# Kernel tuning notes

Measured on AMD Instinct MI355X. Metric: run time of the kernel, lower is better.

The kernel has to match this reference:

```python
import jax, jax.numpy as jnp
import numpy as np

B, C, H, W = 16, 256, 64, 64

def setup_inputs() -> dict:
    key = jax.random.key(0)
    ks = jax.random.split(key, 4)
    scale = 1.0 / np.sqrt(C)
    return {
        "x": jax.random.normal(ks[0], (B, C, H, W), dtype=jnp.float32),
        "w1": jax.random.normal(ks[1], (C, C), dtype=jnp.float32) * scale,
        "b1": jnp.zeros((C,), dtype=jnp.float32),
        "w2": jax.random.normal(ks[2], (C, C), dtype=jnp.float32) * scale,
        "b2": jnp.zeros((C,), dtype=jnp.float32),
        "w3": jax.random.normal(ks[3], (C, C), dtype=jnp.float32) * scale,
        "b3": jnp.zeros((C,), dtype=jnp.float32),
    }

def reference(x, w1, b1, w2, b2, w3, b3):
    b, c, h, w = x.shape
    n = h * w
    # 1x1 convs == per-pixel linear maps over channels; w has shape [C_out, C_in]
    def proj(wt, bias):
        return jnp.einsum('bchw,oc->bohw', x, wt) + bias[None, :, None, None]
    v = proj(w1, b1).reshape(b, c, n).transpose(0, 2, 1)   # [B, N, C]
    q = proj(w2, b2).reshape(b, c, n)                      # [B, C, N]
    k = proj(w3, b3).reshape(b, c, n)                      # [B, C, N]
    weight = jnp.einsum('bcn,bdn->bcd', q, k)              # [B, C, C]
    # global softmax over the entire flattened C*C matrix per batch element
    weight = jax.nn.softmax(weight.reshape(b, -1), axis=1).reshape(b, c, c)
    out = jnp.einsum('bnc,bcd->bdn', v, weight)            # [B, C, N]
    return out.reshape(x.shape)
```

## Files before the change

### kernel.cpp

```cpp
#include <hip/hip_runtime.h>


typedef unsigned short u16;
typedef __attribute__((ext_vector_type(8))) short short8;
typedef __attribute__((ext_vector_type(4))) float floatx4;

__device__ __forceinline__ u16 f2b(float f) {
  union { float f; unsigned int u; } v; v.f = f;
  unsigned int u = v.u;
  return (u16)((u + 0x7fffu + ((u >> 16) & 1u)) >> 16);
}
__device__ __forceinline__ float b2f(u16 h) {
  union { unsigned int u; float f; } v; v.u = ((unsigned int)h) << 16;
  return v.f;
}
__device__ __forceinline__ unsigned int cvt_pk_bf16(float lo, float hi) {
  unsigned int r;
  asm("v_cvt_pk_bf16_f32 %0, %1, %2" : "=v"(r) : "v"(lo), "v"(hi));
  return r;
}
__device__ __forceinline__ void gload_lds16(const u16* g, u16* l) {
  __builtin_amdgcn_global_load_lds(
      (const __attribute__((address_space(1))) unsigned int*)(const void*)g,
      (__attribute__((address_space(3))) unsigned int*)(void*)l, 16, 0, 0);
}

__global__ __launch_bounds__(256) void prep_w_kernel(
    const float* __restrict__ w1, const float* __restrict__ w2, const float* __restrict__ w3,
    u16* __restrict__ W1Th, u16* __restrict__ W2h, u16* __restrict__ W2l,
    u16* __restrict__ W3h, u16* __restrict__ W3l, float* __restrict__ xsum) {
  const int blk = blockIdx.x, t = threadIdx.x;
  if (blk == 576) {
#pragma unroll
    for (int i = 0; i < 16; ++i) xsum[t + i * 256] = 0.f;
    return;
  }
  if (blk < 64) {
    __shared__ float tile[32][33];
    const int e0 = (blk & 7) * 32, c0 = (blk >> 3) * 32;
    const int tx = t & 31, ty = t >> 5;
#pragma unroll
    for (int i = 0; i < 4; ++i)
      tile[ty + i * 8][tx] = w1[(c0 + ty + i * 8) * 256 + e0 + tx];
    __syncthreads();
#pragma unroll
    for (int i = 0; i < 4; ++i)
      W1Th[(e0 + ty + i * 8) * 256 + c0 + tx] = f2b(tile[tx][ty + i * 8]);
  } else {
    const int i = (blk - 64) * 256 + t;
    const int e = i & 0xffff;
    const float f = (i >> 16) ? w3[e] : w2[e];
    u16 h = f2b(f);
    if (i >> 16) { W3h[e] = h; W3l[e] = f2b(f - b2f(h)); }
    else         { W2h[e] = h; W2l[e] = f2b(f - b2f(h)); }
  }
}

__device__ __forceinline__ void stage8(const float4 a, const float4 b,
                                       u16* dH, u16* dL, float& xa) {
  const float f[8] = {a.x, a.y, a.z, a.w, b.x, b.y, b.z, b.w};
  union { unsigned int w[4]; uint4 q; } uh, ul;
#pragma unroll
  for (int i = 0; i < 4; ++i) {
    const unsigned int h = cvt_pk_bf16(f[2 * i], f[2 * i + 1]);
    uh.w[i] = h;
    union { unsigned int u; float ff; } h0, h1;
    h0.u = h << 16;
    h1.u = h & 0xffff0000u;
    ul.w[i] = cvt_pk_bf16(f[2 * i] - h0.ff, f[2 * i + 1] - h1.ff);
    xa += f[2 * i] + f[2 * i + 1];
  }
  *(uint4*)dH = uh.q;
  *(uint4*)dL = ul.q;
}

__global__ __launch_bounds__(512, 4) void gram_kernel(
    const float* __restrict__ x, float* __restrict__ Gp, float* __restrict__ xsum) {
  __shared__ u16 lH[2][256 * 32], lL[2][256 * 32];
  const int b = blockIdx.x >> 5, s = (blockIdx.x >> 1) & 15, mh = blockIdx.x & 1;
  const float* Xb = x + (long)b * 1048576 + s * 256;
  const int t = threadIdx.x;
  const int lane = t & 63, wave = t >> 6;
  const int quad = lane >> 4, l16 = lane & 15;
  const int wml = (wave & 1) * 64 + mh * 128;
  const int wn = (wave >> 1) * 64;
  const int r0 = t >> 2, qc = (t & 3) * 8;
  const int r1 = r0 + 128;
  const int wq = (((t & 3) ^ ((r0 >> 1) & 3))) * 8;
  const int rq = ((quad ^ ((l16 >> 1) & 3))) * 8;
  const int ph = s & 7;
  floatx4 acc[4][4] = {};
  float xa0 = 0.f, xa1 = 0.f;
  float4 p[4];
  {
    const long k0 = ph * 32;
    p[0] = *(const float4*)(Xb + (long)r0 * 4096 + k0 + qc);
    p[1] = *(const float4*)(Xb + (long)r0 * 4096 + k0 + qc + 4);
    p[2] = *(const float4*)(Xb + (long)r1 * 4096 + k0 + qc);
    p[3] = *(const float4*)(Xb + (long)r1 * 4096 + k0 + qc + 4);
  }
  stage8(p[0], p[1], lH[0] + r0 * 32 + wq, lL[0] + r0 * 32 + wq, xa0);
  stage8(p[2], p[3], lH[0] + r1 * 32 + wq, lL[0] + r1 * 32 + wq, xa1);
  __syncthreads();
  for (int kb = 0; kb < 8; ++kb) {
    const int cur = kb & 1, nxt = cur ^ 1;
    if (kb < 7) {
      const long kk = (long)(((kb + 1 + ph) & 7) * 32);
      p[0] = *(const float4*)(Xb + (long)r0 * 4096 + kk + qc);
      p[1] = *(const float4*)(Xb + (long)r0 * 4096 + kk + qc + 4);
      p[2] = *(const float4*)(Xb + (long)r1 * 4096 + kk + qc);
      p[3] = *(const float4*)(Xb + (long)r1 * 4096 + kk + qc + 4);
    }
    const u16* cH = lH[cur];
    const u16* cL = lL[cur];
    short8 ah[4], al[4];
#pragma unroll
    for (int i = 0; i < 4; ++i) {
      ah[i] = *(const short8*)(cH + (wml + i * 16 + l16) * 32 + rq);
      al[i] = *(const short8*)(cL + (wml + i * 16 + l16) * 32 + rq);
    }
#pragma unroll
    for (int j = 0; j < 4; ++j) {
      const short8 bh = *(const short8*)(cH + (wn + j * 16 + l16) * 32 + rq);
      const short8 bl = *(const short8*)(cL + (wn + j * 16 + l16) * 32 + rq);
#pragma unroll
      for (int i = 0; i < 4; ++i) {
        acc[i][j] = __builtin_amdgcn_mfma_f32_16x16x32_bf16(ah[i], bh, acc[i][j], 0, 0, 0);
        acc[i][j] = __builtin_amdgcn_mfma_f32_16x16x32_bf16(ah[i], bl, acc[i][j], 0, 0, 0);
        acc[i][j] = __builtin_amdgcn_mfma_f32_16x16x32_bf16(al[i], bh, acc[i][j], 0, 0, 0);
      }
    }
    if (kb < 7) {
      stage8(p[0], p[1], lH[nxt] + r0 * 32 + wq, lL[nxt] + r0 * 32 + wq, xa0);
      stage8(p[2], p[3], lH[nxt] + r1 * 32 + wq, lL[nxt] + r1 * 32 + wq, xa1);
    }
    __syncthreads();
  }
  if (mh == 0) {
    float v = xa0;
    v += __shfl_xor(v, 1);
    v += __shfl_xor(v, 2);
    if ((t & 3) == 0) atomicAdd(&xsum[b * 256 + r0], v);
    v = xa1;
    v += __shfl_xor(v, 1);
    v += __shfl_xor(v, 2);
    if ((t & 3) == 0) atomicAdd(&xsum[b * 256 + r1], v);
  }
  float* G = Gp + ((long)b * 16 + s) * 65536;
#pragma unroll
  for (int i = 0; i < 4; ++i) {
    const int row0 = wml + i * 16 + quad * 4;
#pragma unroll
    for (int j = 0; j < 4; ++j) {
      const int col = wn + j * 16 + l16;
#pragma unroll
      for (int r = 0; r < 4; ++r)
        G[(long)(row0 + r) * 256 + col] = acc[i][j][r];
    }
  }
}

__global__ __launch_bounds__(256) void reduce_g_kernel(
    const float* __restrict__ Gp, u16* __restrict__ Gh, u16* __restrict__ Gl) {
  const long e = ((long)blockIdx.x * 256 + threadIdx.x) * 4;
  const long base = ((e >> 16) << 20) + (e & 65535);
  float4 s = {0.f, 0.f, 0.f, 0.f};
#pragma unroll
  for (int i = 0; i < 16; ++i) {
    const float4 v = *(const float4*)(Gp + base + (long)i * 65536);
    s.x += v.x; s.y += v.y; s.z += v.z; s.w += v.w;
  }
  union { u16 h[4]; uint2 q; } oh, ol;
  const float sv[4] = {s.x, s.y, s.z, s.w};
#pragma unroll
  for (int c = 0; c < 4; ++c) {
    const u16 h = f2b(sv[c]);
    oh.h[c] = h;
    ol.h[c] = f2b(sv[c] - b2f(h));
  }
  *(uint2*)(Gh + e) = oh.q;
  *(uint2*)(Gl + e) = ol.q;
}

template <bool X3, int EPI>
__global__ __launch_bounds__(256) void gemm_small(
    const u16* __restrict__ Ah, const u16* __restrict__ Al,
    const u16* __restrict__ Bh, const u16* __restrict__ Bl,
    long aBatch, long bBatch, long oBatch,
    float* __restrict__ outF, u16* __restrict__ outH, u16* __restrict__ outL,
    const float* __restrict__ S2, const float* __restrict__ S3,
    const float* __restrict__ b2v, const float* __restrict__ b3v,
    float* __restrict__ bm, float* __restrict__ bs) {
  constexpr int LW = 264;
  __shared__ u16 smem[(X3 ? 4 : 2) * 64 * LW];
  __shared__ float rm[4], rs[4];
  u16* lAh = smem;
  u16* lBh = smem + 64 * LW;
  u16* lAl = X3 ? (smem + 2 * 64 * LW) : nullptr;
  u16* lBl = X3 ? (smem + 3 * 64 * LW) : nullptr;
  const int b = blockIdx.z;
  const int tm = blockIdx.x & 3, tn = blockIdx.x >> 2;
  const u16* Ahb = Ah + (long)b * aBatch + (long)tm * 64 * 256;
  const u16* Bhb = Bh + (long)b * bBatch + (long)tn * 64 * 256;
  const int t = threadIdx.x;
  const int lane = t & 63, wave = t >> 6;
  const int quad = lane >> 4, l16 = lane & 15;
  const int wm = (wave & 1) * 32, wn = (wave >> 1) * 32;
  const int r = t >> 2, c4 = t & 3;
  {
    uint4 tmp[8];
#pragma unroll
    for (int j = 0; j < 8; ++j)
      tmp[j] = *(const uint4*)(Ahb + (long)r * 256 + (c4 + 4 * j) * 8);
#pragma unroll
    for (int j = 0; j < 8; ++j)
      *(uint4*)(lAh + r * LW + (c4 + 4 * j) * 8) = tmp[j];
#pragma unroll
    for (int j = 0; j < 8; ++j)
      tmp[j] = *(const uint4*)(Bhb + (long)r * 256 + (c4 + 4 * j) * 8);
#pragma unroll
    for (int j = 0; j < 8; ++j)
      *(uint4*)(lBh + r * LW + (c4 + 4 * j) * 8) = tmp[j];
    if (X3) {
      const u16* Alb = Al + (long)b * aBatch + (long)tm * 64 * 256;
      const u16* Blb = Bl + (long)b * bBatch + (long)tn * 64 * 256;
#pragma unroll
      for (int j = 0; j < 8; ++j)
        tmp[j] = *(const uint4*)(Alb + (long)r * 256 + (c4 + 4 * j) * 8);
#pragma unroll
      for (int j = 0; j < 8; ++j)
        *(uint4*)(lAl + r * LW + (c4 + 4 * j) * 8) = tmp[j];
#pragma unroll
      for (int j = 0; j < 8; ++j)
        tmp[j] = *(const uint4*)(Blb + (long)r * 256 + (c4 + 4 * j) * 8);
#pragma unroll
      for (int j = 0; j < 8; ++j)
        *(uint4*)(lBl + r * LW + (c4 + 4 * j) * 8) = tmp[j];
    }
  }
  __syncthreads();
  floatx4 acc[2][2] = {};
#pragma unroll
  for (int kk = 0; kk < 8; ++kk) {
    const int co = kk * 32 + quad * 8;
    short8 afh[2], bfh[2];
#pragma unroll
    for (int i = 0; i < 2; ++i) {
      afh[i] = *(const short8*)(lAh + (wm + i * 16 + l16) * LW + co);
      bfh[i] = *(const short8*)(lBh + (wn + i * 16 + l16) * LW + co);
    }
    if (X3) {
      short8 afl[2], bfl[2];
#pragma unroll
      for (int i = 0; i < 2; ++i) {
        afl[i] = *(const short8*)(lAl + (wm + i * 16 + l16) * LW + co);
        bfl[i] = *(const short8*)(lBl + (wn + i * 16 + l16) * LW + co);
      }
#pragma unroll
      for (int i = 0; i < 2; ++i)
#pragma unroll
        for (int j = 0; j < 2; ++j) {
          acc[i][j] = __builtin_amdgcn_mfma_f32_16x16x32_bf16(afh[i], bfh[j], acc[i][j], 0, 0, 0);
          acc[i][j] = __builtin_amdgcn_mfma_f32_16x16x32_bf16(afh[i], bfl[j], acc[i][j], 0, 0, 0);
          acc[i][j] = __builtin_amdgcn_mfma_f32_16x16x32_bf16(afl[i], bfh[j], acc[i][j], 0, 0, 0);
        }
    } else {
#pragma unroll
      for (int i = 0; i < 2; ++i)
#pragma unroll
        for (int j = 0; j < 2; ++j)
          acc[i][j] = __builtin_amdgcn_mfma_f32_16x16x32_bf16(afh[i], bfh[j], acc[i][j], 0, 0, 0);
    }
  }
  const long obase = (long)b * oBatch;
  if (EPI == 3) {
    float vals[2][2][4];
    float vmax = -3.4e38f;
#pragma unroll
    for (int i = 0; i < 2; ++i) {
      const int mb = tm * 64 + wm + i * 16 + quad * 4;
#pragma unroll
      for (int rr = 0; rr < 4; ++rr) {
        const int d = mb + rr;
        const float c1 = b3v[d];
        const float c0 = S3[b * 256 + d] + 4096.f * c1;
#pragma unroll
        for (int j = 0; j < 2; ++j) {
          const int a = tn * 64 + wn + j * 16 + l16;
          const float raw = acc[i][j][rr];
          const float vv = raw + b2v[a] * c0 + c1 * S2[b * 256 + a];
          vals[i][j][rr] = vv;
          vmax = fmaxf(vmax, vv);
          outF[obase + (long)d * 256 + a] = raw;
        }
      }
    }
    for (int o = 32; o; o >>= 1) vmax = fmaxf(vmax, __shfl_xor(vmax, o));
    if (lane == 0) rm[wave] = vmax;
    __syncthreads();
    const float bmax = fmaxf(fmaxf(rm[0], rm[1]), fmaxf(rm[2], rm[3]));
    float se = 0.f;
#pragma unroll
    for (int i = 0; i < 2; ++i)
#pragma unroll
      for (int j = 0; j < 2; ++j)
#pragma unroll
        for (int rr = 0; rr < 4; ++rr) se += __expf(vals[i][j][rr] - bmax);
    for (int o = 32; o; o >>= 1) se += __shfl_xor(se, o);
    if (lane == 0) rs[wave] = se;
    __syncthreads();
    if (t == 0) {
      bm[b * 16 + blockIdx.x] = bmax;
      bs[b * 16 + blockIdx.x] = rs[0] + rs[1] + rs[2] + rs[3];
    }
    return;
  }
#pragma unroll
  for (int i = 0; i < 2; ++i) {
    const int mb = tm * 64 + wm + i * 16 + quad * 4;
#pragma unroll
    for (int j = 0; j < 2; ++j) {
      const int n = tn * 64 + wn + j * 16 + l16;
#pragma unroll
      for (int rr = 0; rr < 4; ++rr) {
        const float v = acc[i][j][rr];
        const long idx = obase + (long)(mb + rr) * 256 + n;
        if (EPI == 0) {
          outF[idx] = v;
        } else if (EPI == 1) {
          u16 h = f2b(v);
          outH[idx] = h;
          outL[idx] = f2b(v - b2f(h));
        } else {
          outH[idx] = f2b(v);
        }
      }
    }
  }
}

__global__ __launch_bounds__(512, 2) void gemm_out(
    const u16* __restrict__ Mh, const float* __restrict__ x,
    const float* __restrict__ bb, float* __restrict__ out) {
  __shared__ u16 lA[2][256 * 32];
  __shared__ u16 lB[128 * 40];
  const int b = blockIdx.z;
  const int tn = blockIdx.x;
  const u16* Ab = Mh + (long)b * 65536;
  const float* Xb = x + (long)b * 1048576 + tn * 128;
  const int t = threadIdx.x;
  const int lane = t & 63, wave = t >> 6;
  const int quad = lane >> 4, l16 = lane & 15;
  const int wm = (wave & 3) * 64;
  const int wn = (wave >> 2) * 64;
  const int erp = (t >> 5) * 2;
  const int n0 = t & 31;
  const int ra = t >> 2;
  const int sc = ((t & 3) ^ ((t >> 3) & 3)) * 8;
  const int rqA = (quad ^ ((l16 >> 1) & 3)) * 8;
  u16* wA0 = &lA[0][0] + wave * 16 * 32;
  u16* wA1 = &lA[1][0] + wave * 16 * 32;
  floatx4 acc[4][4] = {};
  float pb[8];
  gload_lds16(Ab + (long)ra * 256 + sc, wA0);
  gload_lds16(Ab + (long)(ra + 128) * 256 + sc, wA0 + 128 * 32);
#pragma unroll
  for (int i = 0; i < 4; ++i) {
    pb[i]     = Xb[(long)erp * 4096 + n0 + 32 * i];
    pb[4 + i] = Xb[(long)(erp + 1) * 4096 + n0 + 32 * i];
  }
  for (int s = 0; s < 8; ++s) {
    const int kk = s * 32;
    const u16* curA = lA[s & 1];
    __syncthreads();
#pragma unroll
    for (int i = 0; i < 4; ++i) {
      const int nl = n0 + 32 * i;
      const int sb = (erp >> 3) ^ ((nl >> 4) & 3);
      *(unsigned int*)(lB + nl * 40 + sb * 8 + (erp & 7)) =
          cvt_pk_bf16(pb[i], pb[4 + i]);
    }
    __syncthreads();
    if (s < 7) {
      const int k2 = kk + 32;
      u16* nA = (s & 1) ? wA0 : wA1;
      gload_lds16(Ab + (long)ra * 256 + k2 + sc, nA);
      gload_lds16(Ab + (long)(ra + 128) * 256 + k2 + sc, nA + 128 * 32);
#pragma unroll
      for (int i = 0; i < 4; ++i) {
        pb[i]     = Xb[(long)(k2 + erp) * 4096 + n0 + 32 * i];
        pb[4 + i] = Xb[(long)(k2 + erp + 1) * 4096 + n0 + 32 * i];
      }
    }
    short8 af[4];
#pragma unroll
    for (int i = 0; i < 4; ++i)
      af[i] = *(const short8*)(curA + (wm + i * 16 + l16) * 32 + rqA);
#pragma unroll
    for (int j = 0; j < 4; ++j) {
      const int n = wn + j * 16 + l16;
      const int rb = quad ^ ((n >> 4) & 3);
      const short8 bf = *(const short8*)(lB + n * 40 + rb * 8);
#pragma unroll
      for (int i = 0; i < 4; ++i)
        acc[i][j] = __builtin_amdgcn_mfma_f32_16x16x32_bf16(af[i], bf, acc[i][j], 0, 0, 0);
    }
  }
  const long obase = (long)b * 1048576;
#pragma unroll
  for (int i = 0; i < 4; ++i) {
    const int mb = wm + i * 16 + quad * 4;
#pragma unroll
    for (int j = 0; j < 4; ++j) {
      const int n = tn * 128 + wn + j * 16 + l16;
#pragma unroll
      for (int r = 0; r < 4; ++r)
        out[obase + (long)(mb + r) * 4096 + n] = acc[i][j][r] + bb[b * 256 + mb + r];
    }
  }
}

__global__ __launch_bounds__(512) void bias_prep_kernel(
    const float* __restrict__ w2, const float* __restrict__ w3,
    const float* __restrict__ xsum, float* __restrict__ S2, float* __restrict__ S3) {
  __shared__ float xs[256];
  const int b = blockIdx.x, t = threadIdx.x;
  if (t < 256) xs[t] = xsum[b * 256 + t];
  __syncthreads();
  const float* wm = (t < 256) ? w2 : w3;
  const int a = t & 255;
  float s = 0.f;
#pragma unroll 4
  for (int c = 0; c < 256; ++c) s += wm[a * 256 + c] * xs[c];
  if (t < 256) S2[b * 256 + a] = s;
  else         S3[b * 256 + a] = s;
}

__global__ __launch_bounds__(256) void softmax_pass3(
    const float* __restrict__ Lt, const float* __restrict__ S2, const float* __restrict__ S3,
    const float* __restrict__ b2, const float* __restrict__ b3,
    const float* __restrict__ bm, const float* __restrict__ bs,
    const float* __restrict__ b1, u16* __restrict__ WTh, float* __restrict__ bb) {
  __shared__ float ls2[256], lb2[256], lb1[256];
  __shared__ float sM, sInv;
  const int b = blockIdx.y, blk = blockIdx.x, t = threadIdx.x;
  if (t < 64) {
    const float m = (t < 16) ? bm[b * 16 + t] : -3.4e38f;
    float s = (t < 16) ? bs[b * 16 + t] : 0.f;
    float M = m;
    for (int o = 32; o; o >>= 1) M = fmaxf(M, __shfl_xor(M, o));
    s *= __expf(m - M);
    for (int o = 32; o; o >>= 1) s += __shfl_xor(s, o);
    if (t == 0) { sM = M; sInv = 1.0f / s; }
  }
  ls2[t] = S2[b * 256 + t];
  lb2[t] = b2[t];
  lb1[t] = b1[t];
  __syncthreads();
  const float M = sM, inv = sInv;
  const int fw0 = blk * 2048 + t * 8;
  const int d = fw0 >> 8, a0 = fw0 & 255;
  const float c1 = b3[d];
  const float c0 = S3[b * 256 + d] + 4096.f * c1;
  const long base = (long)b * 65536 + fw0;
  float4 v0 = *(const float4*)(Lt + base);
  float4 v1 = *(const float4*)(Lt + base + 4);
  float v[8] = {v0.x, v0.y, v0.z, v0.w, v1.x, v1.y, v1.z, v1.w};
  union { u16 h[8]; uint4 q; } o;
  float bsum = 0.f;
#pragma unroll
  for (int i = 0; i < 8; ++i) {
    const float vv = v[i] + lb2[a0 + i] * c0 + c1 * ls2[a0 + i];
    const float w = __expf(vv - M) * inv;
    o.h[i] = f2b(w);
    bsum += w * lb1[a0 + i];
  }
  *(uint4*)(WTh + base) = o.q;
  for (int off = 16; off; off >>= 1) bsum += __shfl_xor(bsum, off);
  if ((t & 31) == 0) bb[b * 256 + d] = bsum;
}

extern "C" void kernel_launch(void* const* d_in, const int* in_sizes, int n_in,
                              void* d_out, int out_size, void* d_ws, size_t ws_size,
                              hipStream_t stream) {
  const float* x  = (const float*)d_in[0];
  const float* w1 = (const float*)d_in[1];
  const float* b1 = (const float*)d_in[2];
  const float* w2 = (const float*)d_in[3];
  const float* b2 = (const float*)d_in[4];
  const float* w3 = (const float*)d_in[5];
  const float* b3 = (const float*)d_in[6];
  float* out = (float*)d_out;

  char* ws = (char*)d_ws;
  size_t off = 0;
  auto alloc = [&](size_t bytes) {
    void* p = ws + off;
    off += (bytes + 255) & ~(size_t)255;
    return p;
  };
  float* Gp = (float*)alloc(16ull * 16 * 65536 * 4);
  float* xsum = (float*)alloc(16 * 256 * 4);
  u16* Gh   = (u16*)alloc(16ull * 65536 * 2);
  u16* Gl   = (u16*)alloc(16ull * 65536 * 2);
  u16* T3h  = (u16*)alloc(16ull * 65536 * 2);
  u16* T3l  = (u16*)alloc(16ull * 65536 * 2);
  float* Lb = (float*)alloc(16ull * 65536 * 4);
  u16* WTh  = (u16*)alloc(16ull * 65536 * 2);
  u16* Mh   = (u16*)alloc(16ull * 65536 * 2);
  u16* W1Th = (u16*)alloc(65536 * 2);
  u16* W2h  = (u16*)alloc(65536 * 2);
  u16* W2l  = (u16*)alloc(65536 * 2);
  u16* W3h  = (u16*)alloc(65536 * 2);
  u16* W3l  = (u16*)alloc(65536 * 2);
  float* S2   = (float*)alloc(16 * 256 * 4);
  float* S3   = (float*)alloc(16 * 256 * 4);
  float* bmx  = (float*)alloc(16 * 16 * 4);
  float* bsx  = (float*)alloc(16 * 16 * 4);
  float* bb   = (float*)alloc(16 * 256 * 4);

  prep_w_kernel<<<577, 256, 0, stream>>>(w1, w2, w3, W1Th, W2h, W2l, W3h, W3l, xsum);

  gram_kernel<<<512, 512, 0, stream>>>(x, Gp, xsum);
  reduce_g_kernel<<<1024, 256, 0, stream>>>(Gp, Gh, Gl);

  bias_prep_kernel<<<16, 512, 0, stream>>>(w2, w3, xsum, S2, S3);

  gemm_small<true, 1><<<dim3(16, 1, 16), 256, 0, stream>>>(
      W3h, W3l, Gh, Gl, 0, 65536, 65536, nullptr, T3h, T3l,
      nullptr, nullptr, nullptr, nullptr, nullptr, nullptr);
  gemm_small<true, 3><<<dim3(16, 1, 16), 256, 0, stream>>>(
      T3h, T3l, W2h, W2l, 65536, 0, 65536, Lb, nullptr, nullptr,
      S2, S3, b2, b3, bmx, bsx);

  softmax_pass3<<<dim3(32, 16), 256, 0, stream>>>(Lb, S2, S3, b2, b3, bmx, bsx,
                                                  b1, WTh, bb);

  gemm_small<false, 2><<<dim3(16, 1, 16), 256, 0, stream>>>(
      WTh, nullptr, W1Th, nullptr, 65536, 0, 65536, nullptr, Mh, nullptr,
      nullptr, nullptr, nullptr, nullptr, nullptr, nullptr);
  gemm_out<<<dim3(32, 1, 16), 512, 0, stream>>>(Mh, x, bb, out);
}
```

Baseline: 213.2 us.

## Prefetch gram tiles two stages ahead and merge bias prep into reduce

In the gram kernel, global loads for the next K tile are issued right after staging into LDS, so they overlap the following MFMA block and the barrier instead of being issued at the top of each iteration. Separately, the bias-prep work (w2/w3 times xsum) is folded into the G-reduction kernel as 16 extra blocks, removing one kernel launch. The merged kernel makes each bias block compute both S2 and S3 serially with 256 threads, so those blocks run longer than before.

After: 320.7 us. 50.5% more time.

```diff
diff --git a/kernel.cpp b/kernel.cpp
--- a/kernel.cpp
+++ b/kernel.cpp
@@ -93,7 +93,7 @@
   float xa0 = 0.f, xa1 = 0.f;
   float4 p[4];
   {
-    const long k0 = ph * 32;
+    const long k0 = (long)(ph * 32);
     p[0] = *(const float4*)(Xb + (long)r0 * 4096 + k0 + qc);
     p[1] = *(const float4*)(Xb + (long)r0 * 4096 + k0 + qc + 4);
     p[2] = *(const float4*)(Xb + (long)r1 * 4096 + k0 + qc);
@@ -101,16 +101,16 @@
   }
   stage8(p[0], p[1], lH[0] + r0 * 32 + wq, lL[0] + r0 * 32 + wq, xa0);
   stage8(p[2], p[3], lH[0] + r1 * 32 + wq, lL[0] + r1 * 32 + wq, xa1);
+  {
+    const long k1 = (long)(((1 + ph) & 7) * 32);
+    p[0] = *(const float4*)(Xb + (long)r0 * 4096 + k1 + qc);
+    p[1] = *(const float4*)(Xb + (long)r0 * 4096 + k1 + qc + 4);
+    p[2] = *(const float4*)(Xb + (long)r1 * 4096 + k1 + qc);
+    p[3] = *(const float4*)(Xb + (long)r1 * 4096 + k1 + qc + 4);
+  }
   __syncthreads();
   for (int kb = 0; kb < 8; ++kb) {
     const int cur = kb & 1, nxt = cur ^ 1;
-    if (kb < 7) {
-      const long kk = (long)(((kb + 1 + ph) & 7) * 32);
-      p[0] = *(const float4*)(Xb + (long)r0 * 4096 + kk + qc);
-      p[1] = *(const float4*)(Xb + (long)r0 * 4096 + kk + qc + 4);
-      p[2] = *(const float4*)(Xb + (long)r1 * 4096 + kk + qc);
-      p[3] = *(const float4*)(Xb + (long)r1 * 4096 + kk + qc + 4);
-    }
     const u16* cH = lH[cur];
     const u16* cL = lL[cur];
     short8 ah[4], al[4];
@@ -133,6 +133,13 @@
     if (kb < 7) {
       stage8(p[0], p[1], lH[nxt] + r0 * 32 + wq, lL[nxt] + r0 * 32 + wq, xa0);
       stage8(p[2], p[3], lH[nxt] + r1 * 32 + wq, lL[nxt] + r1 * 32 + wq, xa1);
+      if (kb < 6) {
+        const long kk = (long)(((kb + 2 + ph) & 7) * 32);
+        p[0] = *(const float4*)(Xb + (long)r0 * 4096 + kk + qc);
+        p[1] = *(const float4*)(Xb + (long)r0 * 4096 + kk + qc + 4);
+        p[2] = *(const float4*)(Xb + (long)r1 * 4096 + kk + qc);
+        p[3] = *(const float4*)(Xb + (long)r1 * 4096 + kk + qc + 4);
+      }
     }
     __syncthreads();
   }
@@ -160,26 +167,44 @@
   }
 }
 
-__global__ __launch_bounds__(256) void reduce_g_kernel(
-    const float* __restrict__ Gp, u16* __restrict__ Gh, u16* __restrict__ Gl) {
-  const long e = ((long)blockIdx.x * 256 + threadIdx.x) * 4;
-  const long base = ((e >> 16) << 20) + (e & 65535);
-  float4 s = {0.f, 0.f, 0.f, 0.f};
-#pragma unroll
-  for (int i = 0; i < 16; ++i) {
-    const float4 v = *(const float4*)(Gp + base + (long)i * 65536);
-    s.x += v.x; s.y += v.y; s.z += v.z; s.w += v.w;
-  }
-  union { u16 h[4]; uint2 q; } oh, ol;
-  const float sv[4] = {s.x, s.y, s.z, s.w};
-#pragma unroll
-  for (int c = 0; c < 4; ++c) {
-    const u16 h = f2b(sv[c]);
-    oh.h[c] = h;
-    ol.h[c] = f2b(sv[c] - b2f(h));
-  }
-  *(uint2*)(Gh + e) = oh.q;
-  *(uint2*)(Gl + e) = ol.q;
+__global__ __launch_bounds__(256) void reduce_bias_kernel(
+    const float* __restrict__ Gp, u16* __restrict__ Gh, u16* __restrict__ Gl,
+    const float* __restrict__ w2, const float* __restrict__ w3,
+    const float* __restrict__ xsum, float* __restrict__ S2, float* __restrict__ S3) {
+  __shared__ float xs[256];
+  const int t = threadIdx.x;
+  if (blockIdx.x < 1024) {
+    const long e = ((long)blockIdx.x * 256 + t) * 4;
+    const long base = ((e >> 16) << 20) + (e & 65535);
+    float4 s = {0.f, 0.f, 0.f, 0.f};
+#pragma unroll
+    for (int i = 0; i < 16; ++i) {
+      const float4 v = *(const float4*)(Gp + base + (long)i * 65536);
+      s.x += v.x; s.y += v.y; s.z += v.z; s.w += v.w;
+    }
+    union { u16 h[4]; uint2 q; } oh, ol;
+    const float sv[4] = {s.x, s.y, s.z, s.w};
+#pragma unroll
+    for (int c = 0; c < 4; ++c) {
+      const u16 h = f2b(sv[c]);
+      oh.h[c] = h;
+      ol.h[c] = f2b(sv[c] - b2f(h));
+    }
+    *(uint2*)(Gh + e) = oh.q;
+    *(uint2*)(Gl + e) = ol.q;
+  } else {
+    const int b = blockIdx.x - 1024;
+    xs[t] = xsum[b * 256 + t];
+    __syncthreads();
+    float s2 = 0.f, s3 = 0.f;
+#pragma unroll 4
+    for (int c = 0; c < 256; ++c) {
+      s2 += w2[t * 256 + c] * xs[c];
+      s3 += w3[t * 256 + c] * xs[c];
+    }
+    S2[b * 256 + t] = s2;
+    S3[b * 256 + t] = s3;
+  }
 }
 
 template <bool X3, int EPI>
@@ -420,22 +445,6 @@
   }
 }
 
-__global__ __launch_bounds__(512) void bias_prep_kernel(
-    const float* __restrict__ w2, const float* __restrict__ w3,
-    const float* __restrict__ xsum, float* __restrict__ S2, float* __restrict__ S3) {
-  __shared__ float xs[256];
-  const int b = blockIdx.x, t = threadIdx.x;
-  if (t < 256) xs[t] = xsum[b * 256 + t];
-  __syncthreads();
-  const float* wm = (t < 256) ? w2 : w3;
-  const int a = t & 255;
-  float s = 0.f;
-#pragma unroll 4
-  for (int c = 0; c < 256; ++c) s += wm[a * 256 + c] * xs[c];
-  if (t < 256) S2[b * 256 + a] = s;
-  else         S3[b * 256 + a] = s;
-}
-
 __global__ __launch_bounds__(256) void softmax_pass3(
     const float* __restrict__ Lt, const float* __restrict__ S2, const float* __restrict__ S3,
     const float* __restrict__ b2, const float* __restrict__ b3,
@@ -522,9 +531,7 @@
   prep_w_kernel<<<577, 256, 0, stream>>>(w1, w2, w3, W1Th, W2h, W2l, W3h, W3l, xsum);
 
   gram_kernel<<<512, 512, 0, stream>>>(x, Gp, xsum);
-  reduce_g_kernel<<<1024, 256, 0, stream>>>(Gp, Gh, Gl);
-
-  bias_prep_kernel<<<16, 512, 0, stream>>>(w2, w3, xsum, S2, S3);
+  reduce_bias_kernel<<<1040, 256, 0, stream>>>(Gp, Gh, Gl, w2, w3, xsum, S2, S3);
 
   gemm_small<true, 1><<<dim3(16, 1, 16), 256, 0, stream>>>(
       W3h, W3l, Gh, Gl, 0, 65536, 65536, nullptr, T3h, T3l,
```
